# Kernel tuning notes

Hardware: AMD Instinct MI355X
Metric: run time of the kernel (lower is better)

Reference implementation:

```python
import jax, jax.numpy as jnp
import numpy as np

B, N, H, W = 2, 2048, 256, 256
C = 128
STATE = 256
FEAT_IN = C + 2
MID = 6  # layer_num - 2 residual blocks
OUT_DIM = 2


def setup_inputs() -> dict:
    key = jax.random.key(0)
    ks = jax.random.split(key, 8)
    s = 0.01  # matches nn.Linear init normal_(0.0, 0.01)
    features = jax.random.normal(ks[0], (B, C, H, W), jnp.float32)
    base_point = jax.random.uniform(ks[1], (B, N, 2), dtype=jnp.float32)
    adj = jax.random.uniform(ks[2], (B, N, N), dtype=jnp.float32) / N  # row-normalized-ish adjacency
    point_mask = jnp.ones((B, 1, N, 1), jnp.float32)
    w_first = jax.random.normal(ks[3], (2, FEAT_IN, STATE), jnp.float32) * s  # fc1, fc2
    b_first = jnp.zeros((2, STATE), jnp.float32)
    w_mid = jax.random.normal(ks[4], (MID, 4, STATE, STATE), jnp.float32) * s  # per block: gcn1.fc1, gcn1.fc2, gcn2.fc1, gcn2.fc2
    b_mid = jnp.zeros((MID, 4, STATE), jnp.float32)
    w_last = jax.random.normal(ks[5], (2, STATE, STATE), jnp.float32) * s
    b_last = jnp.zeros((2, STATE), jnp.float32)
    w_fc = jax.random.normal(ks[6], (STATE, OUT_DIM), jnp.float32) * s
    b_fc = jnp.zeros((OUT_DIM,), jnp.float32)
    return dict(features=features, base_point=base_point, adj=adj, point_mask=point_mask,
                w_first=w_first, b_first=b_first, w_mid=w_mid, b_mid=b_mid,
                w_last=w_last, b_last=b_last, w_fc=w_fc, b_fc=b_fc)


def _interp(feat, coords, h, w):
    # feat: [B, H*W, C]; coords: [B, N, 2] in [0,1] (x, y order as in torch code)
    Xs = coords[:, :, 0] * w
    Ys = coords[:, :, 1] * h
    X0f = jnp.floor(Xs); X1f = X0f + 1.0
    Y0f = jnp.floor(Ys); Y1f = Y0f + 1.0
    w00 = (X1f - Xs) * (Y1f - Ys)
    w01 = (X1f - Xs) * (Ys - Y0f)
    w10 = (Xs - X0f) * (Y1f - Ys)
    w11 = (Xs - X0f) * (Ys - Y0f)
    X0 = jnp.clip(X0f, 0, w - 1).astype(jnp.int32)
    X1 = jnp.clip(X1f, 0, w - 1).astype(jnp.int32)
    Y0 = jnp.clip(Y0f, 0, h - 1).astype(jnp.int32)
    Y1 = jnp.clip(Y1f, 0, h - 1).astype(jnp.int32)
    def gather(idx):  # idx: [B, N] -> [B, N, C]
        return jnp.take_along_axis(feat, idx[:, :, None], axis=1)
    m00 = gather(X0 + Y0 * w)
    m01 = gather(X0 + Y1 * w)
    m10 = gather(X1 + Y0 * w)
    m11 = gather(X1 + Y1 * w)
    return (w00[..., None] * m00 + w01[..., None] * m01 +
            w10[..., None] * m10 + w11[..., None] * m11)


def _gconv(x, adj, w1, b1, w2, b2):
    # GraphConvolution: fc1(x) + fc2(adj @ x)
    return (x @ w1 + b1) + (jnp.matmul(adj, x) @ w2 + b2)


def _res_block(x, adj, w, b):
    h = jax.nn.relu(_gconv(x, adj, w[0], b[0], w[1], b[1]))
    h = _gconv(h, adj, w[2], b[2], w[3], b[3])
    return jax.nn.relu(h + x)


def _forward(features, base_point, adj, point_mask,
             w_first, b_first, w_mid, b_mid, w_last, b_last, w_fc, b_fc):
    b, c, h, w = features.shape
    feat_flat = features.reshape(b, c, h * w).transpose(0, 2, 1)  # [B, HW, C]
    cnn_feature = _interp(feat_flat, base_point, h, w)            # [B, N, C]
    x = jnp.concatenate([cnn_feature, base_point], axis=2)        # [B, N, C+2]
    x = _gconv(x, adj, w_first[0], b_first[0], w_first[1], b_first[1])
    for i in range(MID):
        x = _res_block(x, adj, w_mid[i], b_mid[i])
    x = _gconv(x, adj, w_last[0], b_last[0], w_last[1], b_last[1])
    gcn_pred = x @ w_fc + b_fc                                    # [B, N, out_dim]
    mask = point_mask.squeeze(1)                                  # [B, N, 1]
    pred_points = base_point + gcn_pred[:, :, :2] * mask
    lap1 = base_point - jnp.matmul(adj, base_point)
    lap2 = pred_points - jnp.matmul(adj, pred_points)
    lap_energy = jnp.sqrt((((lap2 - lap1) ** 2) + 1e-10).sum(-1)).mean(-1)  # [B]
    return pred_points, gcn_pred, lap_energy


def reference(features, base_point, adj, point_mask,
              w_first, b_first, w_mid, b_mid, w_last, b_last, w_fc, b_fc):
    return _forward(features, base_point, adj, point_mask,
                    w_first, b_first, w_mid, b_mid, w_last, b_last, w_fc, b_fc)
```

## Files before the change

kernel.cpp:

```cpp
#include <hip/hip_runtime.h>
#include <hip/hip_bf16.h>
#include <math.h>

#define BB 2
#define NN 2048
#define HH 256
#define WW 256
#define CC 128
#define MIDN 6

typedef __hip_bfloat16 bf16;
typedef short short8 __attribute__((ext_vector_type(8)));
typedef float f32x4 __attribute__((ext_vector_type(4)));
typedef unsigned short ushort4v __attribute__((ext_vector_type(4)));

__device__ inline float bf2f(unsigned short u) {
    return __uint_as_float(((unsigned int)u) << 16);
}
__device__ inline unsigned short f2bf_bits(float f) {
    __hip_bfloat16 h = __float2bfloat16(f);
    return *reinterpret_cast<unsigned short*>(&h);
}

__global__ void prep_kernel(const float* __restrict__ adj, bf16* __restrict__ adjB,
                            const float* __restrict__ features, const float* __restrict__ base_point,
                            bf16* __restrict__ x0p,
                            const float* __restrict__ w_first, const float* __restrict__ w_mid,
                            const float* __restrict__ w_last, bf16* __restrict__ wT) {
    __shared__ float tbuf[32][33];
    int bid = blockIdx.x;
    int t = threadIdx.x;
    if (bid < 4096) {
        size_t i = ((size_t)bid * 256 + t) * 8;
        float4 f0 = *(const float4*)(adj + i);
        float4 f1 = *(const float4*)(adj + i + 4);
        short8 v;
        v[0] = (short)f2bf_bits(f0.x); v[1] = (short)f2bf_bits(f0.y);
        v[2] = (short)f2bf_bits(f0.z); v[3] = (short)f2bf_bits(f0.w);
        v[4] = (short)f2bf_bits(f1.x); v[5] = (short)f2bf_bits(f1.y);
        v[6] = (short)f2bf_bits(f1.z); v[7] = (short)f2bf_bits(f1.w);
        *(short8*)(adjB + i) = v;
    } else if (bid < 8192) {
        int idx = bid - 4096;
        int b   = idx >> 11;
        float xs = base_point[idx * 2 + 0] * (float)WW;
        float ys = base_point[idx * 2 + 1] * (float)HH;
        float x0f = floorf(xs), y0f = floorf(ys);
        float x1f = x0f + 1.f, y1f = y0f + 1.f;
        float w00 = (x1f - xs) * (y1f - ys);
        float w01 = (x1f - xs) * (ys - y0f);
        float w10 = (xs - x0f) * (y1f - ys);
        float w11 = (xs - x0f) * (ys - y0f);
        int X0 = (int)fminf(fmaxf(x0f, 0.f), (float)(WW - 1));
        int X1 = (int)fminf(fmaxf(x1f, 0.f), (float)(WW - 1));
        int Y0 = (int)fminf(fmaxf(y0f, 0.f), (float)(HH - 1));
        int Y1 = (int)fminf(fmaxf(y1f, 0.f), (float)(HH - 1));
        int p00 = Y0 * WW + X0, p01 = Y1 * WW + X0;
        int p10 = Y0 * WW + X1, p11 = Y1 * WW + X1;
        float val = 0.f;
        if (t < CC) {
            const float* f = features + (size_t)(b * CC + t) * (HH * WW);
            val = w00 * f[p00] + w01 * f[p01] + w10 * f[p10] + w11 * f[p11];
        } else if (t == CC) {
            val = base_point[idx * 2 + 0];
        } else if (t == CC + 1) {
            val = base_point[idx * 2 + 1];
        }
        x0p[(size_t)idx * 256 + t] = __float2bfloat16(val);
    } else {
        int idx = bid - 8192;
        int m   = idx >> 6;
        int sub = idx & 63;
        int bx = sub & 7, by = sub >> 3;
        const float* S; int R;
        if (m < 2)       { S = w_first + (size_t)m * 130 * 256; R = 130; }
        else if (m < 26) { S = w_mid + (size_t)(m - 2) * 65536; R = 256; }
        else             { S = w_last + (size_t)(m - 26) * 65536; R = 256; }
        bf16* D = wT + (size_t)m * 65536;
        int tx = t & 31, ty = t >> 5;
        int c0 = bx * 32, r0 = by * 32;
        #pragma unroll
        for (int k = 0; k < 4; ++k) {
            int r = r0 + ty + 8 * k;
            tbuf[ty + 8 * k][tx] = (r < R) ? S[(size_t)r * 256 + c0 + tx] : 0.f;
        }
        __syncthreads();
        #pragma unroll
        for (int k = 0; k < 4; ++k) {
            int c = c0 + ty + 8 * k;
            D[(size_t)c * 256 + r0 + tx] = __float2bfloat16(tbuf[tx][ty + 8 * k]);
        }
    }
}

__global__ __launch_bounds__(256) void s_kernel(const bf16* __restrict__ gprev,
                                                const bf16* __restrict__ v0,
                                                const bf16* __restrict__ v1,
                                                const float* __restrict__ bias1,
                                                const float* __restrict__ bias2,
                                                const bf16* __restrict__ res,
                                                int relu,
                                                const bf16* __restrict__ wcat,
                                                bf16* __restrict__ xR,
                                                bf16* __restrict__ g1out,
                                                bf16* __restrict__ g2T) {
    __shared__ bf16 Al[32 * 64];
    __shared__ bf16 Bl[128 * 64];
    int tid = threadIdx.x;
    int ct = blockIdx.x, rt = blockIdx.y;
    int lane = tid & 63, w = tid >> 6;
    int wr = w >> 1, wc = w & 1;
    int row16 = lane & 15, kg = lane >> 4;
    f32x4 acc[4] = {};
    for (int it = 0; it < 4; ++it) {
        {
            int d = tid * 16;
            int row = d >> 7;
            int cb = d & 127;
            int gcol = it * 64 + (cb >> 1);
            int ridx = rt * 32 + row;
            short8 gv = *(const short8*)(gprev + (size_t)ridx * 256 + gcol);
            short8 pk;
            if (v0) {
                short8 a0 = *(const short8*)(v0 + (size_t)ridx * 256 + gcol);
                short8 a1 = *(const short8*)(v1 + (size_t)ridx * 256 + gcol);
                short8 rv = {};
                if (res) rv = *(const short8*)(res + (size_t)ridx * 256 + gcol);
                #pragma unroll
                for (int j = 0; j < 8; ++j) {
                    float f = bf2f((unsigned short)gv[j]) + bf2f((unsigned short)a0[j])
                            + bf2f((unsigned short)a1[j]) + bias1[gcol + j] + bias2[gcol + j];
                    if (res)  f += bf2f((unsigned short)rv[j]);
                    if (relu) f = fmaxf(f, 0.f);
                    pk[j] = (short)f2bf_bits(f);
                }
            } else {
                pk = gv;
            }
            if (ct == 0) *(short8*)(xR + (size_t)ridx * 256 + gcol) = pk;
            int byte = row * 128 + (cb ^ ((row & 7) << 4));
            *(short8*)((char*)Al + byte) = pk;
        }
        #pragma unroll
        for (int rnd = 0; rnd < 4; ++rnd) {
            int d = tid * 16 + rnd * 4096;
            int row = d >> 7;
            int cb = d & 127;
            int sc = (cb ^ ((row & 7) << 4)) >> 1;
            __builtin_amdgcn_global_load_lds(
                (const __attribute__((address_space(1))) void*)(wcat + (size_t)(ct * 128 + row) * 256 + it * 64 + sc),
                (__attribute__((address_space(3))) void*)((char*)Bl + (w << 10) + rnd * 4096),
                16, 0, 0);
        }
        asm volatile("s_waitcnt vmcnt(0)" ::: "memory");
        __syncthreads();
        #pragma unroll
        for (int kk = 0; kk < 2; ++kk) {
            int arow = wr * 16 + row16;
            int abyte = arow * 128 + (((kk * 64) + kg * 16) ^ ((arow & 7) << 4));
            short8 a = *(const short8*)((const char*)Al + abyte);
            #pragma unroll
            for (int nf = 0; nf < 4; ++nf) {
                int fr = wc * 64 + nf * 16 + row16;
                int byte = fr * 128 + (((kk * 64) + kg * 16) ^ ((fr & 7) << 4));
                short8 bfr = *(const short8*)((const char*)Bl + byte);
                acc[nf] = __builtin_amdgcn_mfma_f32_16x16x32_bf16(a, bfr, acc[nf], 0, 0, 0);
            }
        }
        __syncthreads();
    }
    int cbase = ct * 128 + wc * 64;
    int rb = rt * 32 + wr * 16 + kg * 4;
    if (cbase < 256) {
        #pragma unroll
        for (int nf = 0; nf < 4; ++nf) {
            int c = cbase + nf * 16 + row16;
            #pragma unroll
            for (int j = 0; j < 4; ++j)
                *reinterpret_cast<unsigned short*>(&g1out[(size_t)(rb + j) * 256 + c]) = f2bf_bits(acc[nf][j]);
        }
    } else {
        #pragma unroll
        for (int nf = 0; nf < 4; ++nf) {
            int c = cbase - 256 + nf * 16 + row16;
            ushort4v pk;
            #pragma unroll
            for (int j = 0; j < 4; ++j) pk[j] = f2bf_bits(acc[nf][j]);
            *(ushort4v*)(g2T + (size_t)c * 4096 + rb) = pk;
        }
    }
}

__global__ __launch_bounds__(256) void adjb_kernel(const bf16* __restrict__ adjB,
                                                   const bf16* __restrict__ g2T,
                                                   bf16* __restrict__ Y0,
                                                   bf16* __restrict__ Y1) {
    __shared__ bf16 Al[64 * 64];
    __shared__ bf16 Bl[64 * 64];
    int tid = threadIdx.x;
    int ct = blockIdx.x, rt = blockIdx.y, bz = blockIdx.z;
    int b = bz >> 1, kh = bz & 1;
    const bf16* Aadj = adjB + (size_t)b * NN * NN + (size_t)(rt * 64) * NN + kh * 1024;
    const bf16* Bg   = g2T + (size_t)(ct * 64) * 4096 + b * NN + kh * 1024;
    bf16* Yo = kh ? Y1 : Y0;
    int lane = tid & 63, w = tid >> 6;
    int wr = w >> 1, wc = w & 1;
    int row16 = lane & 15, kg = lane >> 4;
    f32x4 acc[2][2] = {};
    for (int it = 0; it < 16; ++it) {
        int k0 = it * 64;
        #pragma unroll
        for (int rnd = 0; rnd < 2; ++rnd) {
            int d = tid * 16 + rnd * 4096;
            int row = d >> 7, cb = d & 127;
            int sc = (cb ^ ((row & 7) << 4)) >> 1;
            __builtin_amdgcn_global_load_lds(
                (const __attribute__((address_space(1))) void*)(Aadj + (size_t)row * NN + k0 + sc),
                (__attribute__((address_space(3))) void*)((char*)Al + (w << 10) + rnd * 4096),
                16, 0, 0);
        }
        #pragma unroll
        for (int rnd = 0; rnd < 2; ++rnd) {
            int d = tid * 16 + rnd * 4096;
            int row = d >> 7, cb = d & 127;
            int sc = (cb ^ ((row & 7) << 4)) >> 1;
            __builtin_amdgcn_global_load_lds(
                (const __attribute__((address_space(1))) void*)(Bg + (size_t)row * 4096 + k0 + sc),
                (__attribute__((address_space(3))) void*)((char*)Bl + (w << 10) + rnd * 4096),
                16, 0, 0);
        }
        asm volatile("s_waitcnt vmcnt(0)" ::: "memory");
        __syncthreads();
        #pragma unroll
        for (int kk = 0; kk < 2; ++kk) {
            short8 a[2], bfr[2];
            #pragma unroll
            for (int mf = 0; mf < 2; ++mf) {
                int row = wr * 32 + mf * 16 + row16;
                int byte = row * 128 + (((kk * 64) + kg * 16) ^ ((row & 7) << 4));
                a[mf] = *(const short8*)((const char*)Al + byte);
            }
            #pragma unroll
            for (int nf = 0; nf < 2; ++nf) {
                int fr = wc * 32 + nf * 16 + row16;
                int byte = fr * 128 + (((kk * 64) + kg * 16) ^ ((fr & 7) << 4));
                bfr[nf] = *(const short8*)((const char*)Bl + byte);
            }
            #pragma unroll
            for (int mf = 0; mf < 2; ++mf)
                #pragma unroll
                for (int nf = 0; nf < 2; ++nf)
                    acc[mf][nf] = __builtin_amdgcn_mfma_f32_16x16x32_bf16(a[mf], bfr[nf], acc[mf][nf], 0, 0, 0);
        }
        __syncthreads();
    }
    #pragma unroll
    for (int mf = 0; mf < 2; ++mf) {
        #pragma unroll
        for (int nf = 0; nf < 2; ++nf) {
            int c  = ct * 64 + wc * 32 + nf * 16 + row16;
            int r0 = b * NN + rt * 64 + wr * 32 + mf * 16 + kg * 4;
            #pragma unroll
            for (int j = 0; j < 4; ++j)
                *reinterpret_cast<unsigned short*>(&Yo[(size_t)(r0 + j) * 256 + c]) = f2bf_bits(acc[mf][nf][j]);
        }
    }
}

__global__ void head_kernel(const bf16* __restrict__ g1, const bf16* __restrict__ Y0,
                            const bf16* __restrict__ Y1, const float* __restrict__ b_last,
                            const float* __restrict__ w_fc, const float* __restrict__ b_fc,
                            const float* __restrict__ base_point, const float* __restrict__ point_mask,
                            float* __restrict__ out, float* __restrict__ dpts) {
    int row = blockIdx.x * 256 + threadIdx.x;
    float s0 = b_fc[0], s1 = b_fc[1];
    for (int d = 0; d < 256; d += 8) {
        short8 a = *(const short8*)(g1 + (size_t)row * 256 + d);
        short8 u = *(const short8*)(Y0 + (size_t)row * 256 + d);
        short8 v = *(const short8*)(Y1 + (size_t)row * 256 + d);
        #pragma unroll
        for (int j = 0; j < 8; ++j) {
            float z = bf2f((unsigned short)a[j]) + bf2f((unsigned short)u[j])
                    + bf2f((unsigned short)v[j]) + b_last[d + j] + b_last[256 + d + j];
            s0 += z * w_fc[(d + j) * 2 + 0];
            s1 += z * w_fc[(d + j) * 2 + 1];
        }
    }
    float m  = point_mask[row];
    float p0 = base_point[row * 2 + 0] + s0 * m;
    float p1 = base_point[row * 2 + 1] + s1 * m;
    out[row * 2 + 0] = p0;
    out[row * 2 + 1] = p1;
    out[2 * BB * NN + row * 2 + 0] = s0;
    out[2 * BB * NN + row * 2 + 1] = s1;
    dpts[row * 2 + 0] = s0 * m;
    dpts[row * 2 + 1] = s1 * m;
}

__global__ void lap_rows(const bf16* __restrict__ adjB, const float* __restrict__ dpts,
                         float* __restrict__ tvals) {
    int w    = threadIdx.x >> 6;
    int lane = threadIdx.x & 63;
    int row  = blockIdx.x * 4 + w;
    int b = row >> 11, n = row & 2047;
    const bf16* ar = adjB + (size_t)b * NN * NN + (size_t)n * NN;
    const float* db = dpts + (size_t)b * NN * 2;
    float s0 = 0.f, s1 = 0.f;
    for (int k4 = 0; k4 < 4; ++k4) {
        int k = k4 * 512 + lane * 8;
        short8 av = *(const short8*)(ar + k);
        #pragma unroll
        for (int j = 0; j < 8; ++j) {
            float a = bf2f((unsigned short)av[j]);
            float2 dv = *(const float2*)(db + (k + j) * 2);
            s0 += a * dv.x;
            s1 += a * dv.y;
        }
    }
    for (int off = 32; off; off >>= 1) {
        s0 += __shfl_xor(s0, off);
        s1 += __shfl_xor(s1, off);
    }
    if (lane == 0) {
        float e0 = dpts[(size_t)row * 2 + 0] - s0;
        float e1 = dpts[(size_t)row * 2 + 1] - s1;
        tvals[row] = sqrtf(e0 * e0 + e1 * e1 + 1e-10f);
    }
}

__global__ void lap_reduce(const float* __restrict__ tvals, float* __restrict__ outp) {
    __shared__ float sd[256];
    int b = blockIdx.x;
    float s = 0.f;
    for (int i = threadIdx.x; i < NN; i += 256) s += tvals[b * NN + i];
    sd[threadIdx.x] = s;
    __syncthreads();
    for (int o = 128; o; o >>= 1) {
        if (threadIdx.x < o) sd[threadIdx.x] += sd[threadIdx.x + o];
        __syncthreads();
    }
    if (threadIdx.x == 0) outp[b] = sd[0] / (float)NN;
}

extern "C" void kernel_launch(void* const* d_in, const int* in_sizes, int n_in,
                              void* d_out, int out_size, void* d_ws, size_t ws_size,
                              hipStream_t stream) {
    const float* features   = (const float*)d_in[0];
    const float* base_point = (const float*)d_in[1];
    const float* adj        = (const float*)d_in[2];
    const float* point_mask = (const float*)d_in[3];
    const float* w_first    = (const float*)d_in[4];
    const float* b_first    = (const float*)d_in[5];
    const float* w_mid      = (const float*)d_in[6];
    const float* b_mid      = (const float*)d_in[7];
    const float* w_last     = (const float*)d_in[8];
    const float* b_last     = (const float*)d_in[9];
    const float* w_fc       = (const float*)d_in[10];
    const float* b_fc       = (const float*)d_in[11];
    float* out = (float*)d_out;
    char* W = (char*)d_ws;

    bf16* adjB   = (bf16*)W;
    bf16* wT     = (bf16*)(W + 16777216);
    bf16* x0p    = (bf16*)(W + 20447232);
    bf16* g1b[2] = { (bf16*)(W + 22544384), (bf16*)(W + 24641536) };
    bf16* g2T    = (bf16*)(W + 26738688);
    bf16* Y0     = (bf16*)(W + 28835840);
    bf16* Y1     = (bf16*)(W + 30932992);
    bf16* xsl[2] = { (bf16*)(W + 33030144), (bf16*)(W + 35127296) };
    bf16* xscr   = (bf16*)(W + 37224448);
    float* dpts  = (float*)(W + 39321600);
    float* tvals = (float*)(W + 39354368);

    prep_kernel<<<9984, 256, 0, stream>>>(adj, adjB, features, base_point, x0p,
                                          w_first, w_mid, w_last, wT);

    dim3 gS(4, 128);
    dim3 gB(4, 32, 4);

    s_kernel<<<gS, 256, 0, stream>>>(x0p, nullptr, nullptr, nullptr, nullptr, nullptr, 0,
                                     wT, xscr, g1b[0], g2T);
    adjb_kernel<<<gB, 256, 0, stream>>>(adjB, g2T, Y0, Y1);

    for (int k = 1; k < 14; ++k) {
        const float *bb1, *bb2;
        const bf16* resp = nullptr;
        bf16* xw;
        int rl;
        if (k == 1) {
            bb1 = b_first; bb2 = b_first + 256; rl = 0; xw = xsl[0];
        } else if ((k & 1) == 0) {
            int m = (k - 2) / 2;
            bb1 = b_mid + (size_t)m * 1024; bb2 = bb1 + 256;
            rl = 1; xw = xscr;
        } else {
            int m = (k - 3) / 2;
            bb1 = b_mid + (size_t)m * 1024 + 512; bb2 = bb1 + 256;
            rl = 1;
            resp = xsl[((k - 3) / 2) & 1];
            xw   = xsl[((k - 1) / 2) & 1];
        }
        s_kernel<<<gS, 256, 0, stream>>>(g1b[(k - 1) & 1], Y0, Y1, bb1, bb2, resp, rl,
                                         wT + (size_t)2 * k * 65536, xw, g1b[k & 1], g2T);
        adjb_kernel<<<gB, 256, 0, stream>>>(adjB, g2T, Y0, Y1);
    }

    head_kernel<<<16, 256, 0, stream>>>(g1b[1], Y0, Y1, b_last, w_fc, b_fc,
                                        base_point, point_mask, out, dpts);
    lap_rows<<<1024, 256, 0, stream>>>(adjB, dpts, tvals);
    lap_reduce<<<BB, 256, 0, stream>>>(tvals, out + 4 * BB * NN);
}
```

Baseline: 376.6 us.

## Retile adjacency GEMM to 128-row tiles with 4-way split-K and XCD-aware block mapping

The adjacency-times-features GEMM now uses 128x64 output tiles with a 4-way split over K instead of 64x64 tiles with a 2-way split. The four partial results are written to separate slices of one buffer and summed by the next s_kernel and by head_kernel. Both GEMM kernels move to a 1D grid whose block index is permuted so neighbouring tiles land on the same XCD for better L2 reuse. The prep kernel also interleaves adjacency conversion blocks with interpolation blocks. In exchange, each layer writes and reads twice as many partial-sum buffers.

After: 339.9 us. -9.7%, faster.

```diff
diff --git a/kernel.cpp b/kernel.cpp
--- a/kernel.cpp
+++ b/kernel.cpp
@@ -8,6 +8,7 @@
 #define WW 256
 #define CC 128
 #define MIDN 6
+#define YSTR 1048576
 
 typedef __hip_bfloat16 bf16;
 typedef short short8 __attribute__((ext_vector_type(8)));
@@ -30,43 +31,46 @@
     __shared__ float tbuf[32][33];
     int bid = blockIdx.x;
     int t = threadIdx.x;
-    if (bid < 4096) {
-        size_t i = ((size_t)bid * 256 + t) * 8;
-        float4 f0 = *(const float4*)(adj + i);
-        float4 f1 = *(const float4*)(adj + i + 4);
-        short8 v;
-        v[0] = (short)f2bf_bits(f0.x); v[1] = (short)f2bf_bits(f0.y);
-        v[2] = (short)f2bf_bits(f0.z); v[3] = (short)f2bf_bits(f0.w);
-        v[4] = (short)f2bf_bits(f1.x); v[5] = (short)f2bf_bits(f1.y);
-        v[6] = (short)f2bf_bits(f1.z); v[7] = (short)f2bf_bits(f1.w);
-        *(short8*)(adjB + i) = v;
-    } else if (bid < 8192) {
-        int idx = bid - 4096;
-        int b   = idx >> 11;
-        float xs = base_point[idx * 2 + 0] * (float)WW;
-        float ys = base_point[idx * 2 + 1] * (float)HH;
-        float x0f = floorf(xs), y0f = floorf(ys);
-        float x1f = x0f + 1.f, y1f = y0f + 1.f;
-        float w00 = (x1f - xs) * (y1f - ys);
-        float w01 = (x1f - xs) * (ys - y0f);
-        float w10 = (xs - x0f) * (y1f - ys);
-        float w11 = (xs - x0f) * (ys - y0f);
-        int X0 = (int)fminf(fmaxf(x0f, 0.f), (float)(WW - 1));
-        int X1 = (int)fminf(fmaxf(x1f, 0.f), (float)(WW - 1));
-        int Y0 = (int)fminf(fmaxf(y0f, 0.f), (float)(HH - 1));
-        int Y1 = (int)fminf(fmaxf(y1f, 0.f), (float)(HH - 1));
-        int p00 = Y0 * WW + X0, p01 = Y1 * WW + X0;
-        int p10 = Y0 * WW + X1, p11 = Y1 * WW + X1;
-        float val = 0.f;
-        if (t < CC) {
-            const float* f = features + (size_t)(b * CC + t) * (HH * WW);
-            val = w00 * f[p00] + w01 * f[p01] + w10 * f[p10] + w11 * f[p11];
-        } else if (t == CC) {
-            val = base_point[idx * 2 + 0];
-        } else if (t == CC + 1) {
-            val = base_point[idx * 2 + 1];
-        }
-        x0p[(size_t)idx * 256 + t] = __float2bfloat16(val);
+    if (bid < 8192) {
+        int sub = bid >> 1;
+        if ((bid & 1) == 0) {
+            size_t i = ((size_t)sub * 256 + t) * 8;
+            float4 f0 = *(const float4*)(adj + i);
+            float4 f1 = *(const float4*)(adj + i + 4);
+            short8 v;
+            v[0] = (short)f2bf_bits(f0.x); v[1] = (short)f2bf_bits(f0.y);
+            v[2] = (short)f2bf_bits(f0.z); v[3] = (short)f2bf_bits(f0.w);
+            v[4] = (short)f2bf_bits(f1.x); v[5] = (short)f2bf_bits(f1.y);
+            v[6] = (short)f2bf_bits(f1.z); v[7] = (short)f2bf_bits(f1.w);
+            *(short8*)(adjB + i) = v;
+        } else {
+            int idx = sub;
+            int b   = idx >> 11;
+            float xs = base_point[idx * 2 + 0] * (float)WW;
+            float ys = base_point[idx * 2 + 1] * (float)HH;
+            float x0f = floorf(xs), y0f = floorf(ys);
+            float x1f = x0f + 1.f, y1f = y0f + 1.f;
+            float w00 = (x1f - xs) * (y1f - ys);
+            float w01 = (x1f - xs) * (ys - y0f);
+            float w10 = (xs - x0f) * (y1f - ys);
+            float w11 = (xs - x0f) * (ys - y0f);
+            int X0 = (int)fminf(fmaxf(x0f, 0.f), (float)(WW - 1));
+            int X1 = (int)fminf(fmaxf(x1f, 0.f), (float)(WW - 1));
+            int Y0 = (int)fminf(fmaxf(y0f, 0.f), (float)(HH - 1));
+            int Y1 = (int)fminf(fmaxf(y1f, 0.f), (float)(HH - 1));
+            int p00 = Y0 * WW + X0, p01 = Y1 * WW + X0;
+            int p10 = Y0 * WW + X1, p11 = Y1 * WW + X1;
+            float val = 0.f;
+            if (t < CC) {
+                const float* f = features + (size_t)(b * CC + t) * (HH * WW);
+                val = w00 * f[p00] + w01 * f[p01] + w10 * f[p10] + w11 * f[p11];
+            } else if (t == CC) {
+                val = base_point[idx * 2 + 0];
+            } else if (t == CC + 1) {
+                val = base_point[idx * 2 + 1];
+            }
+            x0p[(size_t)idx * 256 + t] = __float2bfloat16(val);
+        }
     } else {
         int idx = bid - 8192;
         int m   = idx >> 6;
@@ -94,8 +98,7 @@
 }
 
 __global__ __launch_bounds__(256) void s_kernel(const bf16* __restrict__ gprev,
-                                                const bf16* __restrict__ v0,
-                                                const bf16* __restrict__ v1,
+                                                const bf16* __restrict__ Yb,
                                                 const float* __restrict__ bias1,
                                                 const float* __restrict__ bias2,
                                                 const bf16* __restrict__ res,
@@ -107,7 +110,9 @@
     __shared__ bf16 Al[32 * 64];
     __shared__ bf16 Bl[128 * 64];
     int tid = threadIdx.x;
-    int ct = blockIdx.x, rt = blockIdx.y;
+    int bid = blockIdx.x;
+    int lin = (bid & 7) * 64 + (bid >> 3);
+    int ct = lin & 3, rt = lin >> 2;
     int lane = tid & 63, w = tid >> 6;
     int wr = w >> 1, wc = w & 1;
     int row16 = lane & 15, kg = lane >> 4;
@@ -119,17 +124,24 @@
             int cb = d & 127;
             int gcol = it * 64 + (cb >> 1);
             int ridx = rt * 32 + row;
-            short8 gv = *(const short8*)(gprev + (size_t)ridx * 256 + gcol);
+            size_t off = (size_t)ridx * 256 + gcol;
+            short8 gv = *(const short8*)(gprev + off);
             short8 pk;
-            if (v0) {
-                short8 a0 = *(const short8*)(v0 + (size_t)ridx * 256 + gcol);
-                short8 a1 = *(const short8*)(v1 + (size_t)ridx * 256 + gcol);
+            if (Yb) {
+                float fv[8];
+                #pragma unroll
+                for (int j = 0; j < 8; ++j) fv[j] = bf2f((unsigned short)gv[j]);
+                #pragma unroll
+                for (int p = 0; p < 4; ++p) {
+                    short8 yv = *(const short8*)(Yb + (size_t)p * YSTR + off);
+                    #pragma unroll
+                    for (int j = 0; j < 8; ++j) fv[j] += bf2f((unsigned short)yv[j]);
+                }
                 short8 rv = {};
-                if (res) rv = *(const short8*)(res + (size_t)ridx * 256 + gcol);
+                if (res) rv = *(const short8*)(res + off);
                 #pragma unroll
                 for (int j = 0; j < 8; ++j) {
-                    float f = bf2f((unsigned short)gv[j]) + bf2f((unsigned short)a0[j])
-                            + bf2f((unsigned short)a1[j]) + bias1[gcol + j] + bias2[gcol + j];
+                    float f = fv[j] + bias1[gcol + j] + bias2[gcol + j];
                     if (res)  f += bf2f((unsigned short)rv[j]);
                     if (relu) f = fmaxf(f, 0.f);
                     pk[j] = (short)f2bf_bits(f);
@@ -137,7 +149,7 @@
             } else {
                 pk = gv;
             }
-            if (ct == 0) *(short8*)(xR + (size_t)ridx * 256 + gcol) = pk;
+            if (ct == 0) *(short8*)(xR + off) = pk;
             int byte = row * 128 + (cb ^ ((row & 7) << 4));
             *(short8*)((char*)Al + byte) = pk;
         }
@@ -193,24 +205,25 @@
 
 __global__ __launch_bounds__(256) void adjb_kernel(const bf16* __restrict__ adjB,
                                                    const bf16* __restrict__ g2T,
-                                                   bf16* __restrict__ Y0,
-                                                   bf16* __restrict__ Y1) {
-    __shared__ bf16 Al[64 * 64];
+                                                   bf16* __restrict__ Ybase) {
+    __shared__ bf16 Al[128 * 64];
     __shared__ bf16 Bl[64 * 64];
     int tid = threadIdx.x;
-    int ct = blockIdx.x, rt = blockIdx.y, bz = blockIdx.z;
-    int b = bz >> 1, kh = bz & 1;
-    const bf16* Aadj = adjB + (size_t)b * NN * NN + (size_t)(rt * 64) * NN + kh * 1024;
-    const bf16* Bg   = g2T + (size_t)(ct * 64) * 4096 + b * NN + kh * 1024;
-    bf16* Yo = kh ? Y1 : Y0;
+    int bid = blockIdx.x;
+    int lin = (bid & 7) * 64 + (bid >> 3);
+    int ct = lin & 3, rt = (lin >> 2) & 15, z = lin >> 6;
+    int b = z >> 2, ks = z & 3;
+    const bf16* Aadj = adjB + (size_t)b * NN * NN + (size_t)(rt * 128) * NN + ks * 512;
+    const bf16* Bg   = g2T + (size_t)(ct * 64) * 4096 + b * NN + ks * 512;
+    bf16* Yo = Ybase + (size_t)ks * YSTR;
     int lane = tid & 63, w = tid >> 6;
     int wr = w >> 1, wc = w & 1;
     int row16 = lane & 15, kg = lane >> 4;
-    f32x4 acc[2][2] = {};
-    for (int it = 0; it < 16; ++it) {
+    f32x4 acc[4][2] = {};
+    for (int it = 0; it < 8; ++it) {
         int k0 = it * 64;
         #pragma unroll
-        for (int rnd = 0; rnd < 2; ++rnd) {
+        for (int rnd = 0; rnd < 4; ++rnd) {
             int d = tid * 16 + rnd * 4096;
             int row = d >> 7, cb = d & 127;
             int sc = (cb ^ ((row & 7) << 4)) >> 1;
@@ -233,10 +246,10 @@
         __syncthreads();
         #pragma unroll
         for (int kk = 0; kk < 2; ++kk) {
-            short8 a[2], bfr[2];
-            #pragma unroll
-            for (int mf = 0; mf < 2; ++mf) {
-                int row = wr * 32 + mf * 16 + row16;
+            short8 a[4], bfr[2];
+            #pragma unroll
+            for (int mf = 0; mf < 4; ++mf) {
+                int row = wr * 64 + mf * 16 + row16;
                 int byte = row * 128 + (((kk * 64) + kg * 16) ^ ((row & 7) << 4));
                 a[mf] = *(const short8*)((const char*)Al + byte);
             }
@@ -247,7 +260,7 @@
                 bfr[nf] = *(const short8*)((const char*)Bl + byte);
             }
             #pragma unroll
-            for (int mf = 0; mf < 2; ++mf)
+            for (int mf = 0; mf < 4; ++mf)
                 #pragma unroll
                 for (int nf = 0; nf < 2; ++nf)
                     acc[mf][nf] = __builtin_amdgcn_mfma_f32_16x16x32_bf16(a[mf], bfr[nf], acc[mf][nf], 0, 0, 0);
@@ -255,11 +268,11 @@
         __syncthreads();
     }
     #pragma unroll
-    for (int mf = 0; mf < 2; ++mf) {
+    for (int mf = 0; mf < 4; ++mf) {
         #pragma unroll
         for (int nf = 0; nf < 2; ++nf) {
             int c  = ct * 64 + wc * 32 + nf * 16 + row16;
-            int r0 = b * NN + rt * 64 + wr * 32 + mf * 16 + kg * 4;
+            int r0 = b * NN + rt * 128 + wr * 64 + mf * 16 + kg * 4;
             #pragma unroll
             for (int j = 0; j < 4; ++j)
                 *reinterpret_cast<unsigned short*>(&Yo[(size_t)(r0 + j) * 256 + c]) = f2bf_bits(acc[mf][nf][j]);
@@ -267,21 +280,28 @@
     }
 }
 
-__global__ void head_kernel(const bf16* __restrict__ g1, const bf16* __restrict__ Y0,
-                            const bf16* __restrict__ Y1, const float* __restrict__ b_last,
+__global__ void head_kernel(const bf16* __restrict__ g1, const bf16* __restrict__ Yb,
+                            const float* __restrict__ b_last,
                             const float* __restrict__ w_fc, const float* __restrict__ b_fc,
                             const float* __restrict__ base_point, const float* __restrict__ point_mask,
                             float* __restrict__ out, float* __restrict__ dpts) {
     int row = blockIdx.x * 256 + threadIdx.x;
     float s0 = b_fc[0], s1 = b_fc[1];
     for (int d = 0; d < 256; d += 8) {
-        short8 a = *(const short8*)(g1 + (size_t)row * 256 + d);
-        short8 u = *(const short8*)(Y0 + (size_t)row * 256 + d);
-        short8 v = *(const short8*)(Y1 + (size_t)row * 256 + d);
+        size_t off = (size_t)row * 256 + d;
+        short8 a = *(const short8*)(g1 + off);
+        float zv[8];
+        #pragma unroll
+        for (int j = 0; j < 8; ++j) zv[j] = bf2f((unsigned short)a[j]);
+        #pragma unroll
+        for (int p = 0; p < 4; ++p) {
+            short8 yv = *(const short8*)(Yb + (size_t)p * YSTR + off);
+            #pragma unroll
+            for (int j = 0; j < 8; ++j) zv[j] += bf2f((unsigned short)yv[j]);
+        }
         #pragma unroll
         for (int j = 0; j < 8; ++j) {
-            float z = bf2f((unsigned short)a[j]) + bf2f((unsigned short)u[j])
-                    + bf2f((unsigned short)v[j]) + b_last[d + j] + b_last[256 + d + j];
+            float z = zv[j] + b_last[d + j] + b_last[256 + d + j];
             s0 += z * w_fc[(d + j) * 2 + 0];
             s1 += z * w_fc[(d + j) * 2 + 1];
         }
@@ -365,22 +385,18 @@
     bf16* x0p    = (bf16*)(W + 20447232);
     bf16* g1b[2] = { (bf16*)(W + 22544384), (bf16*)(W + 24641536) };
     bf16* g2T    = (bf16*)(W + 26738688);
-    bf16* Y0     = (bf16*)(W + 28835840);
-    bf16* Y1     = (bf16*)(W + 30932992);
-    bf16* xsl[2] = { (bf16*)(W + 33030144), (bf16*)(W + 35127296) };
-    bf16* xscr   = (bf16*)(W + 37224448);
-    float* dpts  = (float*)(W + 39321600);
-    float* tvals = (float*)(W + 39354368);
+    bf16* Yb     = (bf16*)(W + 28835840);
+    bf16* xsl[2] = { (bf16*)(W + 37224448), (bf16*)(W + 39321600) };
+    bf16* xscr   = (bf16*)(W + 41418752);
+    float* dpts  = (float*)(W + 43515904);
+    float* tvals = (float*)(W + 43548672);
 
     prep_kernel<<<9984, 256, 0, stream>>>(adj, adjB, features, base_point, x0p,
                                           w_first, w_mid, w_last, wT);
 
-    dim3 gS(4, 128);
-    dim3 gB(4, 32, 4);
-
-    s_kernel<<<gS, 256, 0, stream>>>(x0p, nullptr, nullptr, nullptr, nullptr, nullptr, 0,
-                                     wT, xscr, g1b[0], g2T);
-    adjb_kernel<<<gB, 256, 0, stream>>>(adjB, g2T, Y0, Y1);
+    s_kernel<<<512, 256, 0, stream>>>(x0p, nullptr, nullptr, nullptr, nullptr, 0,
+                                      wT, xscr, g1b[0], g2T);
+    adjb_kernel<<<512, 256, 0, stream>>>(adjB, g2T, Yb);
 
     for (int k = 1; k < 14; ++k) {
         const float *bb1, *bb2;
@@ -397,15 +413,15 @@
             int m = (k - 3) / 2;
             bb1 = b_mid + (size_t)m * 1024 + 512; bb2 = bb1 + 256;
             rl = 1;
-            resp = xsl[((k - 3) / 2) & 1];
+            resp = xsl[m & 1];
             xw   = xsl[((k - 1) / 2) & 1];
         }
-        s_kernel<<<gS, 256, 0, stream>>>(g1b[(k - 1) & 1], Y0, Y1, bb1, bb2, resp, rl,
-                                         wT + (size_t)2 * k * 65536, xw, g1b[k & 1], g2T);
-        adjb_kernel<<<gB, 256, 0, stream>>>(adjB, g2T, Y0, Y1);
-    }
-
-    head_kernel<<<16, 256, 0, stream>>>(g1b[1], Y0, Y1, b_last, w_fc, b_fc,
+        s_kernel<<<512, 256, 0, stream>>>(g1b[(k - 1) & 1], Yb, bb1, bb2, resp, rl,
+                                          wT + (size_t)2 * k * 65536, xw, g1b[k & 1], g2T);
+        adjb_kernel<<<512, 256, 0, stream>>>(adjB, g2T, Yb);
+    }
+
+    head_kernel<<<16, 256, 0, stream>>>(g1b[1], Yb, b_last, w_fc, b_fc,
                                         base_point, point_mask, out, dpts);
     lap_rows<<<1024, 256, 0, stream>>>(adjB, dpts, tvals);
     lap_reduce<<<BB, 256, 0, stream>>>(tvals, out + 4 * BB * NN);
```
